# Kernel tuning notes

Measured on AMD Instinct MI355X. Metric: run time of the kernel, lower is better.

## Reference

```python
import jax, jax.numpy as jnp
import numpy as np

SEQ, B = 512, 2048
H, OUT = 512, 1
IN = 32  # linearIn input_size; x feature dim = IN - OUT = 31


def setup_inputs() -> dict:
    key = jax.random.key(0)
    ks = jax.random.split(key, 12)
    u = lambda k, shape, lim: jax.random.uniform(k, shape, jnp.float32, -lim, lim)
    lim_in = 1.0 / np.sqrt(IN)
    lim_h = 1.0 / np.sqrt(H)
    return {
        "x": jax.random.normal(ks[0], (SEQ, B, IN - OUT), jnp.float32),
        # initial states (torch eval path uses randn*0.1)
        "h0": jax.random.normal(ks[1], (B, H), jnp.float32) * 0.1,
        "c0": jax.random.normal(ks[2], (B, H), jnp.float32) * 0.1,
        "y0": jax.random.normal(ks[3], (B, OUT), jnp.float32) * 0.1,
        # linearIn
        "W_in": u(ks[4], (H, IN), lim_in),
        "b_in": u(ks[5], (H,), lim_in),
        # single-layer LSTM (gate order i, f, g, o as in PyTorch)
        "W_ih": u(ks[6], (4 * H, H), lim_h),
        "W_hh": u(ks[7], (4 * H, H), lim_h),
        "b_ih": u(ks[8], (4 * H,), lim_h),
        "b_hh": u(ks[9], (4 * H,), lim_h),
        # linearOut
        "W_out": u(ks[10], (OUT, H), lim_h),
        "b_out": u(ks[11], (OUT,), lim_h),
    }


def reference(x, h0, c0, y0, W_in, b_in, W_ih, W_hh, b_ih, b_hh, W_out, b_out):
    b_gate = b_ih + b_hh

    def step(carry, xt):
        h, c, y = carry  # [B,H], [B,H], [B,OUT]
        inp = jnp.concatenate([xt, y], axis=-1)          # [B, IN]
        x0 = jax.nn.relu(inp @ W_in.T + b_in)            # [B, H]
        gates = x0 @ W_ih.T + h @ W_hh.T + b_gate        # [B, 4H]
        i, f, g, o = jnp.split(gates, 4, axis=-1)
        c = jax.nn.sigmoid(f) * c + jax.nn.sigmoid(i) * jnp.tanh(g)
        h = jax.nn.sigmoid(o) * jnp.tanh(c)
        y = h @ W_out.T + b_out                          # [B, OUT]
        return (h, c, y), y

    _, ys = jax.lax.scan(step, (h0, c0, y0), x)
    return ys  # [SEQ, B, OUT]
```

## Files before the change

### kernel.cpp

```cpp
#include <hip/hip_runtime.h>
#include <hip/hip_bf16.h>
#include <stdint.h>

#define SEQ   512
#define BATCH 2048
#define HID   512
#define XF    31

typedef __bf16 bf16_t;
typedef bf16_t bf16x8 __attribute__((ext_vector_type(8)));
typedef float  f32x4  __attribute__((ext_vector_type(4)));

__device__ __forceinline__ void gload16(const void* g, void* lds) {
    __builtin_amdgcn_global_load_lds(
        (const __attribute__((address_space(1))) void*)g,
        (__attribute__((address_space(3))) void*)lds,
        16, 0, 0);
}

__device__ __forceinline__ float sigmoid_f(float x) {
    return 1.f / (1.f + __expf(-x));
}
__device__ __forceinline__ float tanh_f(float x) {
    float e = __expf(2.f * x);
    return 1.f - 2.f / (e + 1.f);
}

__global__ void prep_w(const float* __restrict__ W_ih, const float* __restrict__ W_hh,
                       bf16_t* __restrict__ Wcat) {
    const int j = blockIdx.x;
    for (int k = threadIdx.x; k < 1024; k += 256) {
        float v = (k < 512) ? W_ih[(size_t)j * 512 + k]
                            : W_hh[(size_t)j * 512 + (k - 512)];
        Wcat[(size_t)j * 1024 + k] = (bf16_t)v;
    }
}

__global__ void prep_state(const float* __restrict__ h0, const float* __restrict__ c0,
                           bf16_t* __restrict__ H0, float* __restrict__ Cbuf) {
    const int b = blockIdx.x;
    for (int d = threadIdx.x; d < 512; d += 256) {
        H0[(size_t)b * 512 + d]   = (bf16_t)h0[(size_t)b * 512 + d];
        Cbuf[(size_t)b * 512 + d] = c0[(size_t)b * 512 + d];
    }
}

__global__ void prep_bias(const float* __restrict__ b_ih, const float* __restrict__ b_hh,
                          float* __restrict__ bg) {
    int j = blockIdx.x * 256 + threadIdx.x;
    bg[j] = b_ih[j] + b_hh[j];
}

__global__ __launch_bounds__(256) void input_proj(
    const float* __restrict__ x_t,
    const float* __restrict__ yprev,
    const float* __restrict__ W_in,
    const float* __restrict__ b_in,
    const float* __restrict__ b_out,
    bf16_t* __restrict__ X0,
    float* __restrict__ yinit)
{
    __shared__ float xs[8][32];
    __shared__ float ys[8];
    const int tid = threadIdx.x;
    const int b0  = blockIdx.x * 8;

    if (tid < 248) {
        int rr = tid / 31, cc = tid % 31;
        xs[rr][cc] = x_t[(size_t)(b0 + rr) * XF + cc];
    } else {
        int rr = tid - 248;
        ys[rr] = yprev[b0 + rr];
        yinit[b0 + rr] = b_out[0];
    }
    __syncthreads();

#pragma unroll
    for (int rep = 0; rep < 2; ++rep) {
        const int hd = tid + rep * 256;
        float wrow[32];
#pragma unroll
        for (int k4 = 0; k4 < 8; ++k4) {
            float4 v = *(const float4*)&W_in[(size_t)hd * 32 + k4 * 4];
            wrow[k4 * 4 + 0] = v.x; wrow[k4 * 4 + 1] = v.y;
            wrow[k4 * 4 + 2] = v.z; wrow[k4 * 4 + 3] = v.w;
        }
        const float bi = b_in[hd];
#pragma unroll
        for (int b = 0; b < 8; ++b) {
            float acc = bi + ys[b] * wrow[31];
#pragma unroll
            for (int k = 0; k < 31; ++k) acc += xs[b][k] * wrow[k];
            acc = fmaxf(acc, 0.f);
            X0[(size_t)(b0 + b) * 512 + hd] = (bf16_t)acc;
        }
    }
}

__global__ __launch_bounds__(512, 1) void step_gemm_cell(
    const bf16_t* __restrict__ X0,
    const bf16_t* __restrict__ Hin,
    bf16_t* __restrict__ Hout,
    float*  __restrict__ Cbuf,
    const bf16_t* __restrict__ Wcat,
    const float*  __restrict__ b_gate,
    const float*  __restrict__ W_out,
    float*  __restrict__ yout)
{
    __shared__ __align__(16) char smem[131072];
    typedef bf16_t Tile[128][64];
    Tile* As = (Tile*)smem;
    Tile* Bs = (Tile*)(smem + 65536);
    float (*Gs0)[128] = (float (*)[128])smem;
    float (*Gs1)[128] = (float (*)[128])(smem + 65536);

    const int tid  = threadIdx.x;
    const int lane = tid & 63;
    const int wid  = tid >> 6;
    const int wm   = wid >> 2;
    const int wn   = (wid >> 1) & 1;
    const int wk   = wid & 1;

    const int bid  = blockIdx.x;
    const int xcd  = bid & 7;
    const int slot = bid >> 3;
    const int xm   = xcd >> 1;
    const int xn   = xcd & 1;
    const int mb   = xm * 4 + (slot & 3);
    const int nb   = xn * 8 + (slot >> 2);

    const int r  = lane & 15, q = lane >> 4;
    const int lr  = lane >> 3;
    const int lcs = ((lane & 7) ^ lr) * 8;
    const int ko  = (((wk << 2) + q) ^ (r & 7)) << 3;

    f32x4 acc[4][4];
#pragma unroll
    for (int mi = 0; mi < 4; ++mi)
#pragma unroll
        for (int ni = 0; ni < 4; ++ni) {
            f32x4 z = {0.f, 0.f, 0.f, 0.f};
            acc[mi][ni] = z;
        }

    auto stage = [&](int dst, int kt) {
        const bf16_t* abase = (kt < 8) ? X0 : Hin;
        const int k0 = (kt & 7) * 64;
#pragma unroll
        for (int iss = 0; iss < 2; ++iss) {
            const int r0 = wid * 16 + iss * 8;
            gload16(abase + (size_t)(mb * 128 + r0 + lr) * 512 + k0 + lcs,
                    &As[dst][r0][0]);
        }
#pragma unroll
        for (int iss = 0; iss < 2; ++iss) {
            const int r0   = wid * 16 + iss * 8;
            const int nloc = r0 + lr;
            const int j    = (nloc >> 5) * 512 + nb * 32 + (nloc & 31);
            gload16(Wcat + (size_t)j * 1024 + kt * 64 + lcs,
                    &Bs[dst][r0][0]);
        }
    };

    stage(0, 0);
    stage(1, 1);

#pragma unroll
    for (int kt = 0; kt < 16; ++kt) {
        if (kt + 2 < 16) stage((kt + 2) & 3, kt + 2);
        if (kt < 14) {
            asm volatile("s_waitcnt vmcnt(8)" ::: "memory");
        } else if (kt == 14) {
            asm volatile("s_waitcnt vmcnt(4)" ::: "memory");
        } else {
            asm volatile("s_waitcnt vmcnt(0)" ::: "memory");
        }
        __builtin_amdgcn_s_barrier();
        __builtin_amdgcn_sched_barrier(0);

        const int cur = kt & 3;
        bf16x8 af[4], bfr[4];
#pragma unroll
        for (int mi = 0; mi < 4; ++mi)
            af[mi] = *(const bf16x8*)&As[cur][wm * 64 + mi * 16 + r][ko];
#pragma unroll
        for (int ni = 0; ni < 4; ++ni)
            bfr[ni] = *(const bf16x8*)&Bs[cur][wn * 64 + ni * 16 + r][ko];
#pragma unroll
        for (int mi = 0; mi < 4; ++mi)
#pragma unroll
            for (int ni = 0; ni < 4; ++ni)
                acc[mi][ni] = __builtin_amdgcn_mfma_f32_16x16x32_bf16(
                    af[mi], bfr[ni], acc[mi][ni], 0, 0, 0);
    }

    const int row    = tid >> 2;
    const int dq     = (tid & 3) * 8;
    const int b_glob = mb * 128 + row;

    float cv[8], wo[8];
    *(float4*)&cv[0] = *(const float4*)&Cbuf[(size_t)b_glob * 512 + nb * 32 + dq];
    *(float4*)&cv[4] = *(const float4*)&Cbuf[(size_t)b_glob * 512 + nb * 32 + dq + 4];
    *(float4*)&wo[0] = *(const float4*)&W_out[nb * 32 + dq];
    *(float4*)&wo[4] = *(const float4*)&W_out[nb * 32 + dq + 4];

    __syncthreads();

    {
        float (*G)[128] = wk ? Gs1 : Gs0;
#pragma unroll
        for (int mi = 0; mi < 4; ++mi)
#pragma unroll
            for (int ni = 0; ni < 4; ++ni)
#pragma unroll
                for (int rr = 0; rr < 4; ++rr) {
                    const int gr = wm * 64 + mi * 16 + q * 4 + rr;
                    const int gc = wn * 64 + ni * 16 + r;
                    G[gr][gc ^ ((gr & 7) << 2)] = acc[mi][ni][rr];
                }
    }
    __syncthreads();

    {
        const int sx = (row & 7) << 2;
        float cnew[8];
        bf16_t hv[8];
        float yp = 0.f;
#pragma unroll
        for (int ii = 0; ii < 8; ++ii) {
            const int dl     = dq + ii;
            const int d_glob = nb * 32 + dl;
            const int c0x = (dl)      ^ sx;
            const int c1x = (32 + dl) ^ sx;
            const int c2x = (64 + dl) ^ sx;
            const int c3x = (96 + dl) ^ sx;
            float gi = Gs0[row][c0x] + Gs1[row][c0x] + b_gate[d_glob];
            float gf = Gs0[row][c1x] + Gs1[row][c1x] + b_gate[512  + d_glob];
            float gg = Gs0[row][c2x] + Gs1[row][c2x] + b_gate[1024 + d_glob];
            float go = Gs0[row][c3x] + Gs1[row][c3x] + b_gate[1536 + d_glob];
            float is = sigmoid_f(gi);
            float fs = sigmoid_f(gf);
            float os = sigmoid_f(go);
            float gt = tanh_f(gg);
            float c_new = fs * cv[ii] + is * gt;
            float hval  = os * tanh_f(c_new);
            cnew[ii] = c_new;
            hv[ii]   = (bf16_t)hval;
            yp += hval * wo[ii];
        }
        const size_t base = (size_t)b_glob * 512 + nb * 32 + dq;
        *(float4*)&Cbuf[base]     = *(const float4*)&cnew[0];
        *(float4*)&Cbuf[base + 4] = *(const float4*)&cnew[4];
        *(bf16x8*)&Hout[base]     = *(const bf16x8*)&hv[0];

        yp += __shfl_xor(yp, 1);
        yp += __shfl_xor(yp, 2);
        if ((tid & 3) == 0) atomicAdd(&yout[b_glob], yp);
    }
}

extern "C" void kernel_launch(void* const* d_in, const int* in_sizes, int n_in,
                              void* d_out, int out_size, void* d_ws, size_t ws_size,
                              hipStream_t stream) {
    const float* x     = (const float*)d_in[0];
    const float* h0    = (const float*)d_in[1];
    const float* c0    = (const float*)d_in[2];
    const float* y0    = (const float*)d_in[3];
    const float* W_in  = (const float*)d_in[4];
    const float* b_in  = (const float*)d_in[5];
    const float* W_ih  = (const float*)d_in[6];
    const float* W_hh  = (const float*)d_in[7];
    const float* b_ih  = (const float*)d_in[8];
    const float* b_hh  = (const float*)d_in[9];
    const float* W_out = (const float*)d_in[10];
    const float* b_out = (const float*)d_in[11];
    float* out = (float*)d_out;

    char* ws = (char*)d_ws;
    bf16_t* Wcat  = (bf16_t*)(ws);
    bf16_t* X0    = (bf16_t*)(ws + (4u << 20));
    bf16_t* Hb0   = (bf16_t*)(ws + (6u << 20));
    bf16_t* Hb1   = (bf16_t*)(ws + (8u << 20));
    float*  Cbuf  = (float*)(ws + (10u << 20));
    float*  bgate = (float*)(ws + (14u << 20));
    bf16_t* Hb[2] = { Hb0, Hb1 };

    prep_w    <<<2048, 256, 0, stream>>>(W_ih, W_hh, Wcat);
    prep_state<<<2048, 256, 0, stream>>>(h0, c0, Hb[0], Cbuf);
    prep_bias <<<8,    256, 0, stream>>>(b_ih, b_hh, bgate);

    for (int t = 0; t < SEQ; ++t) {
        const float* yprev = (t == 0) ? y0 : (out + (size_t)(t - 1) * BATCH);
        input_proj<<<256, 256, 0, stream>>>(
            x + (size_t)t * BATCH * XF, yprev, W_in, b_in, b_out,
            X0, out + (size_t)t * BATCH);
        step_gemm_cell<<<256, 512, 0, stream>>>(
            X0, Hb[t & 1], Hb[(t + 1) & 1], Cbuf, Wcat, bgate, W_out,
            out + (size_t)t * BATCH);
    }
    (void)in_sizes; (void)n_in; (void)out_size; (void)ws_size;
}
```

Measured before the change: 11.54 ms.

## Fuse input projection into LSTM step kernel with split-bf16 MFMA

Removes the separate input_proj launch per timestep by computing the ReLU(W_in·[x,y]+b_in) projection inside the step kernel using MFMA with hi/lo bf16 splitting of both operands, writing X0 directly into LDS instead of global memory. The H·W_hh half of the GEMM runs first, then X0 is built in LDS and the W_ih half follows with a separate double-buffered weight pipeline. Output zeroing moves to a prep kernel and the b_out bias is added via the atomic from nb==0 blocks. This halves kernel launches and drops the X0 global round-trip, at the cost of more LDS (160KB), redundant per-block projection work, and extra barriers.

```diff
diff --git a/kernel.cpp b/kernel.cpp
--- a/kernel.cpp
+++ b/kernel.cpp
@@ -9,6 +9,7 @@
 
 typedef __bf16 bf16_t;
 typedef bf16_t bf16x8 __attribute__((ext_vector_type(8)));
+typedef bf16_t bf16x4 __attribute__((ext_vector_type(4)));
 typedef float  f32x4  __attribute__((ext_vector_type(4)));
 
 __device__ __forceinline__ void gload16(const void* g, void* lds) {
@@ -37,11 +38,13 @@
 }
 
 __global__ void prep_state(const float* __restrict__ h0, const float* __restrict__ c0,
-                           bf16_t* __restrict__ H0, float* __restrict__ Cbuf) {
+                           bf16_t* __restrict__ H0, float* __restrict__ Cbuf,
+                           float* __restrict__ out_all) {
     const int b = blockIdx.x;
     for (int d = threadIdx.x; d < 512; d += 256) {
         H0[(size_t)b * 512 + d]   = (bf16_t)h0[(size_t)b * 512 + d];
         Cbuf[(size_t)b * 512 + d] = c0[(size_t)b * 512 + d];
+        out_all[(size_t)b * 512 + d] = 0.f;
     }
 }
 
@@ -51,66 +54,31 @@
     bg[j] = b_ih[j] + b_hh[j];
 }
 
-__global__ __launch_bounds__(256) void input_proj(
-    const float* __restrict__ x_t,
-    const float* __restrict__ yprev,
-    const float* __restrict__ W_in,
-    const float* __restrict__ b_in,
-    const float* __restrict__ b_out,
-    bf16_t* __restrict__ X0,
-    float* __restrict__ yinit)
-{
-    __shared__ float xs[8][32];
-    __shared__ float ys[8];
-    const int tid = threadIdx.x;
-    const int b0  = blockIdx.x * 8;
-
-    if (tid < 248) {
-        int rr = tid / 31, cc = tid % 31;
-        xs[rr][cc] = x_t[(size_t)(b0 + rr) * XF + cc];
-    } else {
-        int rr = tid - 248;
-        ys[rr] = yprev[b0 + rr];
-        yinit[b0 + rr] = b_out[0];
-    }
-    __syncthreads();
-
-#pragma unroll
-    for (int rep = 0; rep < 2; ++rep) {
-        const int hd = tid + rep * 256;
-        float wrow[32];
-#pragma unroll
-        for (int k4 = 0; k4 < 8; ++k4) {
-            float4 v = *(const float4*)&W_in[(size_t)hd * 32 + k4 * 4];
-            wrow[k4 * 4 + 0] = v.x; wrow[k4 * 4 + 1] = v.y;
-            wrow[k4 * 4 + 2] = v.z; wrow[k4 * 4 + 3] = v.w;
-        }
-        const float bi = b_in[hd];
-#pragma unroll
-        for (int b = 0; b < 8; ++b) {
-            float acc = bi + ys[b] * wrow[31];
-#pragma unroll
-            for (int k = 0; k < 31; ++k) acc += xs[b][k] * wrow[k];
-            acc = fmaxf(acc, 0.f);
-            X0[(size_t)(b0 + b) * 512 + hd] = (bf16_t)acc;
-        }
-    }
-}
-
-__global__ __launch_bounds__(512, 1) void step_gemm_cell(
-    const bf16_t* __restrict__ X0,
+__global__ void prep_wb(const float* __restrict__ W_in,
+                        bf16_t* __restrict__ Wbh, bf16_t* __restrict__ Wbl) {
+    int idx = blockIdx.x * 256 + threadIdx.x;
+    float v = W_in[idx];
+    bf16_t h = (bf16_t)v;
+    Wbh[idx] = h;
+    Wbl[idx] = (bf16_t)(v - (float)h);
+}
+
+__global__ __launch_bounds__(512, 1) void step_fused(
+    const float*  __restrict__ x_t,
+    const float*  __restrict__ yprev,
+    const bf16_t* __restrict__ Wbh,
+    const bf16_t* __restrict__ Wbl,
+    const float*  __restrict__ b_in,
     const bf16_t* __restrict__ Hin,
-    bf16_t* __restrict__ Hout,
-    float*  __restrict__ Cbuf,
+    bf16_t*       __restrict__ Hout,
+    float*        __restrict__ Cbuf,
     const bf16_t* __restrict__ Wcat,
     const float*  __restrict__ b_gate,
     const float*  __restrict__ W_out,
-    float*  __restrict__ yout)
+    const float*  __restrict__ b_out,
+    float*        __restrict__ yout)
 {
-    __shared__ __align__(16) char smem[131072];
-    typedef bf16_t Tile[128][64];
-    Tile* As = (Tile*)smem;
-    Tile* Bs = (Tile*)(smem + 65536);
+    __shared__ __align__(16) char smem[163840];
     float (*Gs0)[128] = (float (*)[128])smem;
     float (*Gs1)[128] = (float (*)[128])(smem + 65536);
 
@@ -124,15 +92,23 @@
     const int bid  = blockIdx.x;
     const int xcd  = bid & 7;
     const int slot = bid >> 3;
-    const int xm   = xcd >> 1;
-    const int xn   = xcd & 1;
-    const int mb   = xm * 4 + (slot & 3);
-    const int nb   = xn * 8 + (slot >> 2);
+    const int mb   = (xcd >> 1) * 4 + (slot & 3);
+    const int nb   = (xcd & 1) * 8 + (slot >> 2);
 
     const int r  = lane & 15, q = lane >> 4;
     const int lr  = lane >> 3;
     const int lcs = ((lane & 7) ^ lr) * 8;
-    const int ko  = (((wk << 2) + q) ^ (r & 7)) << 3;
+    const int kob = (((wk << 2) + q) ^ (r & 7)) * 16;
+
+    const int brow = mb * 128 + wid * 16 + r;
+    float xv[8];
+#pragma unroll
+    for (int j = 0; j < 8; ++j) {
+        const int k = q * 8 + j;
+        const float* ap = (k == 31) ? (yprev + brow)
+                                    : (x_t + (size_t)brow * XF + k);
+        xv[j] = *ap;
+    }
 
     f32x4 acc[4][4];
 #pragma unroll
@@ -143,14 +119,13 @@
             acc[mi][ni] = z;
         }
 
-    auto stage = [&](int dst, int kt) {
-        const bf16_t* abase = (kt < 8) ? X0 : Hin;
-        const int k0 = (kt & 7) * 64;
+    auto stageAB = [&](int dst, int kt) {
+        const int k0 = (kt - 8) * 64;
 #pragma unroll
         for (int iss = 0; iss < 2; ++iss) {
             const int r0 = wid * 16 + iss * 8;
-            gload16(abase + (size_t)(mb * 128 + r0 + lr) * 512 + k0 + lcs,
-                    &As[dst][r0][0]);
+            gload16(Hin + (size_t)(mb * 128 + r0 + lr) * 512 + k0 + lcs,
+                    smem + (size_t)dst * 16384 + r0 * 128);
         }
 #pragma unroll
         for (int iss = 0; iss < 2; ++iss) {
@@ -158,16 +133,25 @@
             const int nloc = r0 + lr;
             const int j    = (nloc >> 5) * 512 + nb * 32 + (nloc & 31);
             gload16(Wcat + (size_t)j * 1024 + kt * 64 + lcs,
-                    &Bs[dst][r0][0]);
+                    smem + 65536 + (size_t)dst * 16384 + r0 * 128);
         }
     };
-
-    stage(0, 0);
-    stage(1, 1);
-
-#pragma unroll
-    for (int kt = 0; kt < 16; ++kt) {
-        if (kt + 2 < 16) stage((kt + 2) & 3, kt + 2);
+    auto stageB2 = [&](int dst, int kt) {
+#pragma unroll
+        for (int iss = 0; iss < 2; ++iss) {
+            const int r0   = wid * 16 + iss * 8;
+            const int nloc = r0 + lr;
+            const int j    = (nloc >> 5) * 512 + nb * 32 + (nloc & 31);
+            gload16(Wcat + (size_t)j * 1024 + kt * 64 + lcs,
+                    smem + 131072 + (size_t)dst * 16384 + r0 * 128);
+        }
+    };
+
+    stageAB(0, 8);
+    stageAB(1, 9);
+#pragma unroll
+    for (int kt = 8; kt < 16; ++kt) {
+        if (kt + 2 < 16) stageAB((kt + 2) & 3, kt + 2);
         if (kt < 14) {
             asm volatile("s_waitcnt vmcnt(8)" ::: "memory");
         } else if (kt == 14) {
@@ -179,19 +163,94 @@
         __builtin_amdgcn_sched_barrier(0);
 
         const int cur = kt & 3;
+        const char* Ab = smem + (size_t)cur * 16384;
+        const char* Bb = smem + 65536 + (size_t)cur * 16384;
         bf16x8 af[4], bfr[4];
 #pragma unroll
         for (int mi = 0; mi < 4; ++mi)
-            af[mi] = *(const bf16x8*)&As[cur][wm * 64 + mi * 16 + r][ko];
+            af[mi] = *(const bf16x8*)(Ab + (wm * 64 + mi * 16 + r) * 128 + kob);
 #pragma unroll
         for (int ni = 0; ni < 4; ++ni)
-            bfr[ni] = *(const bf16x8*)&Bs[cur][wn * 64 + ni * 16 + r][ko];
+            bfr[ni] = *(const bf16x8*)(Bb + (wn * 64 + ni * 16 + r) * 128 + kob);
 #pragma unroll
         for (int mi = 0; mi < 4; ++mi)
 #pragma unroll
             for (int ni = 0; ni < 4; ++ni)
                 acc[mi][ni] = __builtin_amdgcn_mfma_f32_16x16x32_bf16(
                     af[mi], bfr[ni], acc[mi][ni], 0, 0, 0);
+    }
+
+    __syncthreads();
+
+    stageB2(0, 0);
+    stageB2(1, 1);
+
+    bf16x8 xyh, xyl;
+#pragma unroll
+    for (int j = 0; j < 8; ++j) {
+        bf16_t h = (bf16_t)xv[j];
+        xyh[j] = h;
+        xyl[j] = (bf16_t)(xv[j] - (float)h);
+    }
+#pragma unroll
+    for (int dg = 0; dg < 8; ++dg) {
+        bf16x8 wfh[4], wfl[4];
+#pragma unroll
+        for (int u = 0; u < 4; ++u) {
+            const int dt = dg * 4 + u;
+            const size_t wo_ = (size_t)(dt * 16 + r) * 32 + q * 8;
+            wfh[u] = *(const bf16x8*)&Wbh[wo_];
+            wfl[u] = *(const bf16x8*)&Wbl[wo_];
+        }
+#pragma unroll
+        for (int u = 0; u < 4; ++u) {
+            const int dt = dg * 4 + u;
+            f32x4 pa = {0.f, 0.f, 0.f, 0.f};
+            pa = __builtin_amdgcn_mfma_f32_16x16x32_bf16(wfh[u], xyh, pa, 0, 0, 0);
+            pa = __builtin_amdgcn_mfma_f32_16x16x32_bf16(wfh[u], xyl, pa, 0, 0, 0);
+            pa = __builtin_amdgcn_mfma_f32_16x16x32_bf16(wfl[u], xyh, pa, 0, 0, 0);
+            const int d0 = dt * 16 + q * 4;
+            const float4 bi = *(const float4*)&b_in[d0];
+            bf16x4 hv;
+            hv[0] = (bf16_t)fmaxf(pa[0] + bi.x, 0.f);
+            hv[1] = (bf16_t)fmaxf(pa[1] + bi.y, 0.f);
+            hv[2] = (bf16_t)fmaxf(pa[2] + bi.z, 0.f);
+            hv[3] = (bf16_t)fmaxf(pa[3] + bi.w, 0.f);
+            const int c  = dt * 2 + (q >> 1);
+            const int cs = (c & ~7) | ((c & 7) ^ (r & 7));
+            *(bf16x4*)(smem + (size_t)(wid * 16 + r) * 1024 + cs * 16 + (q & 1) * 8) = hv;
+        }
+    }
+
+    __syncthreads();
+
+#pragma unroll
+    for (int kt = 0; kt < 8; ++kt) {
+        if (kt < 7) {
+            asm volatile("s_waitcnt vmcnt(2)" ::: "memory");
+        } else {
+            asm volatile("s_waitcnt vmcnt(0)" ::: "memory");
+        }
+        __builtin_amdgcn_s_barrier();
+        __builtin_amdgcn_sched_barrier(0);
+
+        const char* Bb = smem + 131072 + (size_t)(kt & 1) * 16384;
+        bf16x8 af[4], bfr[4];
+#pragma unroll
+        for (int mi = 0; mi < 4; ++mi)
+            af[mi] = *(const bf16x8*)(smem + (size_t)(wm * 64 + mi * 16 + r) * 1024
+                                      + kt * 128 + kob);
+#pragma unroll
+        for (int ni = 0; ni < 4; ++ni)
+            bfr[ni] = *(const bf16x8*)(Bb + (wn * 64 + ni * 16 + r) * 128 + kob);
+#pragma unroll
+        for (int mi = 0; mi < 4; ++mi)
+#pragma unroll
+            for (int ni = 0; ni < 4; ++ni)
+                acc[mi][ni] = __builtin_amdgcn_mfma_f32_16x16x32_bf16(
+                    af[mi], bfr[ni], acc[mi][ni], 0, 0, 0);
+        __builtin_amdgcn_s_barrier();
+        if (kt + 2 < 8) stageB2(kt & 1, kt + 2);
     }
 
     const int row    = tid >> 2;
@@ -203,6 +262,7 @@
     *(float4*)&cv[4] = *(const float4*)&Cbuf[(size_t)b_glob * 512 + nb * 32 + dq + 4];
     *(float4*)&wo[0] = *(const float4*)&W_out[nb * 32 + dq];
     *(float4*)&wo[4] = *(const float4*)&W_out[nb * 32 + dq + 4];
+    const float bo = b_out[0];
 
     __syncthreads();
 
@@ -255,7 +315,8 @@
 
         yp += __shfl_xor(yp, 1);
         yp += __shfl_xor(yp, 2);
-        if ((tid & 3) == 0) atomicAdd(&yout[b_glob], yp);
+        if ((tid & 3) == 0)
+            atomicAdd(&yout[b_glob], yp + ((nb == 0) ? bo : 0.f));
     }
 }
 
@@ -278,24 +339,24 @@
 
     char* ws = (char*)d_ws;
     bf16_t* Wcat  = (bf16_t*)(ws);
-    bf16_t* X0    = (bf16_t*)(ws + (4u << 20));
-    bf16_t* Hb0   = (bf16_t*)(ws + (6u << 20));
-    bf16_t* Hb1   = (bf16_t*)(ws + (8u << 20));
-    float*  Cbuf  = (float*)(ws + (10u << 20));
-    float*  bgate = (float*)(ws + (14u << 20));
+    bf16_t* Hb0   = (bf16_t*)(ws + (4u << 20));
+    bf16_t* Hb1   = (bf16_t*)(ws + (6u << 20));
+    float*  Cbuf  = (float*)(ws + (8u << 20));
+    float*  bgate = (float*)(ws + (12u << 20));
+    bf16_t* Wbh   = (bf16_t*)(ws + (12u << 20) + (16u << 10));
+    bf16_t* Wbl   = (bf16_t*)(ws + (12u << 20) + (64u << 10));
     bf16_t* Hb[2] = { Hb0, Hb1 };
 
     prep_w    <<<2048, 256, 0, stream>>>(W_ih, W_hh, Wcat);
-    prep_state<<<2048, 256, 0, stream>>>(h0, c0, Hb[0], Cbuf);
+    prep_state<<<2048, 256, 0, stream>>>(h0, c0, Hb[0], Cbuf, out);
     prep_bias <<<8,    256, 0, stream>>>(b_ih, b_hh, bgate);
+    prep_wb   <<<64,   256, 0, stream>>>(W_in, Wbh, Wbl);
 
     for (int t = 0; t < SEQ; ++t) {
         const float* yprev = (t == 0) ? y0 : (out + (size_t)(t - 1) * BATCH);
-        input_proj<<<256, 256, 0, stream>>>(
-            x + (size_t)t * BATCH * XF, yprev, W_in, b_in, b_out,
-            X0, out + (size_t)t * BATCH);
-        step_gemm_cell<<<256, 512, 0, stream>>>(
-            X0, Hb[t & 1], Hb[(t + 1) & 1], Cbuf, Wcat, bgate, W_out,
+        step_fused<<<256, 512, 0, stream>>>(
+            x + (size_t)t * BATCH * XF, yprev, Wbh, Wbl, b_in,
+            Hb[t & 1], Hb[(t + 1) & 1], Cbuf, Wcat, bgate, W_out, b_out,
             out + (size_t)t * BATCH);
     }
     (void)in_sizes; (void)n_in; (void)out_size; (void)ws_size;
```

Result: slower. 12.09 ms (+4.8%).
